# Optimization experiments

Hardware: AMD Instinct MI355X
Metric: run time of the kernel (lower is better)

## Reference

```python
import jax, jax.numpy as jnp
import numpy as np

H = 16   # num_heads
K = 2    # top_k experts per token


def _layer_norm(x, g, b, eps=1e-5):
    mu = jnp.mean(x, axis=-1, keepdims=True)
    var = jnp.mean(jnp.square(x - mu), axis=-1, keepdims=True)
    return (x - mu) * jax.lax.rsqrt(var + eps) * g + b


def setup_inputs() -> dict:
    key = jax.random.key(0)
    ks = jax.random.split(key, 8)
    B, S, D, E = 2, 2048, 1024, 8
    sc = 0.02
    return {
        "x": jax.random.normal(ks[0], (B, S, D), jnp.float32),
        "wq": jax.random.normal(ks[1], (D, D), jnp.float32) * sc,
        "wk": jax.random.normal(ks[2], (D, D), jnp.float32) * sc,
        "wv": jax.random.normal(ks[3], (D, D), jnp.float32) * sc,
        "wo": jax.random.normal(ks[4], (D, D), jnp.float32) * sc,
        "ln1_g": jnp.ones((D,), jnp.float32),
        "ln1_b": jnp.zeros((D,), jnp.float32),
        "ln2_g": jnp.ones((D,), jnp.float32),
        "ln2_b": jnp.zeros((D,), jnp.float32),
        "router_w": jax.random.normal(ks[5], (E, D), jnp.float32) * sc,
        "expert_w": jax.random.normal(ks[6], (E, D, D), jnp.float32) * sc,
    }


def reference(x, wq, wk, wv, wo, ln1_g, ln1_b, ln2_g, ln2_b, router_w, expert_w):
    B, S, D = x.shape
    E = expert_w.shape[0]
    hd = D // H

    # ---- attention sublayer: x = x + attn(norm1(x)) ----
    h = _layer_norm(x, ln1_g, ln1_b)
    q = (h @ wq.T).reshape(B, S, H, hd).transpose(0, 2, 1, 3)  # bhsd
    k = (h @ wk.T).reshape(B, S, H, hd).transpose(0, 2, 1, 3)
    v = (h @ wv.T).reshape(B, S, H, hd).transpose(0, 2, 1, 3)
    scores = jnp.einsum("bhqd,bhkd->bhqk", q, k) / jnp.sqrt(jnp.float32(hd))
    causal = jnp.tril(jnp.ones((S, S), dtype=bool))
    scores = jnp.where(causal, scores, jnp.finfo(scores.dtype).min)
    probs = jax.nn.softmax(scores, axis=-1)
    attn = jnp.einsum("bhqk,bhkd->bhqd", probs, v)
    attn = attn.transpose(0, 2, 1, 3).reshape(B, S, D) @ wo.T
    x = x + attn

    # ---- MoE sublayer: x = x + moe(norm2(x)) ----
    h2 = _layer_norm(x, ln2_g, ln2_b)
    logits = jnp.einsum("bsd,ed->bse", h2, router_w)          # [B,S,E]
    top_logits, top_ids = jax.lax.top_k(logits, K)            # [B,S,K]
    gates = jax.nn.softmax(top_logits, axis=-1)               # [B,S,K]
    # dense combine weights over experts (E is small): sum_k gate_k * onehot(id_k)
    combine = jnp.sum(jax.nn.one_hot(top_ids, E, dtype=h2.dtype) * gates[..., None], axis=-2)  # [B,S,E]
    # per-token matvec with expert weights: token @ W_e.T for each expert, then weighted sum
    y = jnp.einsum("bsd,eod->bseo", h2, expert_w)             # [B,S,E,D]
    moe_out = jnp.einsum("bse,bseo->bso", combine, y)
    return x + moe_out
```

## Files before the change

kernel.cpp:

```cpp
#include <hip/hip_runtime.h>
#include <hip/hip_bf16.h>
#include <cstdint>


typedef __bf16 bf16;
typedef __bf16 bf16x8 __attribute__((ext_vector_type(8)));
typedef __bf16 bf16x4 __attribute__((ext_vector_type(4)));
typedef float f32x4 __attribute__((ext_vector_type(4)));
typedef float f32x16 __attribute__((ext_vector_type(16)));

#define MFMA(a, b, c) __builtin_amdgcn_mfma_f32_16x16x32_bf16(a, b, c, 0, 0, 0)
#define MFMA32(a, b, c) __builtin_amdgcn_mfma_f32_32x32x16_bf16(a, b, c, 0, 0, 0)

__device__ __forceinline__ void gld16(void* lds, const void* g) {
  __builtin_amdgcn_global_load_lds(
      (const __attribute__((address_space(1))) void*)g,
      (__attribute__((address_space(3))) void*)lds, 16, 0, 0);
}

__global__ void prep_weights(const float* __restrict__ wq, const float* __restrict__ wk,
                             const float* __restrict__ wv, const float* __restrict__ wo,
                             const float* __restrict__ expw,
                             bf16* __restrict__ wqh, bf16* __restrict__ wql,
                             bf16* __restrict__ wkh, bf16* __restrict__ wkl,
                             bf16* __restrict__ wvh, bf16* __restrict__ wvl,
                             bf16* __restrict__ woh, bf16* __restrict__ wol,
                             bf16* __restrict__ ewh) {
  int bid = blockIdx.x;
  if (bid < 4096) {
    int wsel = bid >> 10;
    const float* src = wsel == 0 ? wq : wsel == 1 ? wk : wsel == 2 ? wv : wo;
    bf16* hi = wsel == 0 ? wqh : wsel == 1 ? wkh : wsel == 2 ? wvh : woh;
    bf16* lo = wsel == 0 ? wql : wsel == 1 ? wkl : wsel == 2 ? wvl : wol;
    int i = ((bid & 1023) * 256 + threadIdx.x) * 4;
    float4 v = *(const float4*)(src + i);
    float a[4] = {v.x, v.y, v.z, v.w};
#pragma unroll
    for (int j = 0; j < 4; j++) {
      bf16 h = (bf16)a[j];
      hi[i + j] = h;
      lo[i + j] = (bf16)(a[j] - (float)h);
    }
  } else {
    int i = ((bid - 4096) * 256 + threadIdx.x) * 4;
    float4 v = *(const float4*)(expw + i);
    ewh[i] = (bf16)v.x; ewh[i + 1] = (bf16)v.y;
    ewh[i + 2] = (bf16)v.z; ewh[i + 3] = (bf16)v.w;
  }
}

__global__ void ln_split(const float* __restrict__ x, const float* __restrict__ g,
                         const float* __restrict__ b, bf16* __restrict__ hi,
                         bf16* __restrict__ lo) {
  int tok = blockIdx.x, t = threadIdx.x;
  float4 v = ((const float4*)(x + (size_t)tok * 1024))[t];
  float s = v.x + v.y + v.z + v.w;
  float ss = v.x * v.x + v.y * v.y + v.z * v.z + v.w * v.w;
#pragma unroll
  for (int o = 1; o < 64; o <<= 1) { s += __shfl_xor(s, o); ss += __shfl_xor(ss, o); }
  __shared__ float red[8];
  int w = t >> 6, lane = t & 63;
  if (lane == 0) { red[w] = s; red[4 + w] = ss; }
  __syncthreads();
  s = red[0] + red[1] + red[2] + red[3];
  ss = red[4] + red[5] + red[6] + red[7];
  float mu = s * (1.f / 1024.f);
  float rstd = rsqrtf(ss * (1.f / 1024.f) - mu * mu + 1e-5f);
  float4 gv = ((const float4*)g)[t], bv = ((const float4*)b)[t];
  float y[4] = {(v.x - mu) * rstd * gv.x + bv.x, (v.y - mu) * rstd * gv.y + bv.y,
                (v.z - mu) * rstd * gv.z + bv.z, (v.w - mu) * rstd * gv.w + bv.w};
  size_t o = (size_t)tok * 1024 + t * 4;
#pragma unroll
  for (int j = 0; j < 4; j++) {
    bf16 h = (bf16)y[j];
    hi[o + j] = h;
    lo[o + j] = (bf16)(y[j] - (float)h);
  }
}

__global__ void ln2route(const float* __restrict__ x1, const float* __restrict__ g,
                         const float* __restrict__ b, const float* __restrict__ rw,
                         bf16* __restrict__ h2h, int* __restrict__ eid,
                         float2* __restrict__ gout) {
  int tok = blockIdx.x, t = threadIdx.x;
  float4 v = ((const float4*)(x1 + (size_t)tok * 1024))[t];
  float s = v.x + v.y + v.z + v.w;
  float ss = v.x * v.x + v.y * v.y + v.z * v.z + v.w * v.w;
#pragma unroll
  for (int o = 1; o < 64; o <<= 1) { s += __shfl_xor(s, o); ss += __shfl_xor(ss, o); }
  __shared__ float red[8];
  __shared__ float h2s[1024];
  __shared__ float lg[8];
  int w = t >> 6, lane = t & 63;
  if (lane == 0) { red[w] = s; red[4 + w] = ss; }
  __syncthreads();
  s = red[0] + red[1] + red[2] + red[3];
  ss = red[4] + red[5] + red[6] + red[7];
  float mu = s * (1.f / 1024.f);
  float rstd = rsqrtf(ss * (1.f / 1024.f) - mu * mu + 1e-5f);
  float4 gv = ((const float4*)g)[t], bv = ((const float4*)b)[t];
  float4 y;
  y.x = (v.x - mu) * rstd * gv.x + bv.x;
  y.y = (v.y - mu) * rstd * gv.y + bv.y;
  y.z = (v.z - mu) * rstd * gv.z + bv.z;
  y.w = (v.w - mu) * rstd * gv.w + bv.w;
  ((float4*)h2s)[t] = y;
  size_t o = (size_t)tok * 1024 + t * 4;
  h2h[o] = (bf16)y.x; h2h[o + 1] = (bf16)y.y;
  h2h[o + 2] = (bf16)y.z; h2h[o + 3] = (bf16)y.w;
  __syncthreads();
  float a0 = 0.f, a1 = 0.f;
  const float4* r0 = (const float4*)(rw + (2 * w) * 1024);
  const float4* r1 = (const float4*)(rw + (2 * w + 1) * 1024);
#pragma unroll
  for (int it = 0; it < 4; it++) {
    float4 xv = ((const float4*)h2s)[lane + 64 * it];
    float4 w0 = r0[lane + 64 * it];
    float4 w1 = r1[lane + 64 * it];
    a0 += xv.x * w0.x + xv.y * w0.y + xv.z * w0.z + xv.w * w0.w;
    a1 += xv.x * w1.x + xv.y * w1.y + xv.z * w1.z + xv.w * w1.w;
  }
#pragma unroll
  for (int o2 = 1; o2 < 64; o2 <<= 1) {
    a0 += __shfl_xor(a0, o2);
    a1 += __shfl_xor(a1, o2);
  }
  if (lane == 0) { lg[2 * w] = a0; lg[2 * w + 1] = a1; }
  __syncthreads();
  if (t == 0) {
    int i0 = 0; float l0 = lg[0];
#pragma unroll
    for (int e = 1; e < 8; e++) if (lg[e] > l0) { l0 = lg[e]; i0 = e; }
    int i1 = -1; float l1 = -3e38f;
#pragma unroll
    for (int e = 0; e < 8; e++) if (e != i0 && lg[e] > l1) { l1 = lg[e]; i1 = e; }
    float e1 = __expf(l1 - l0);
    float den = 1.f + e1;
    eid[tok] = i0 | (i1 << 4);
    gout[tok] = make_float2(1.f / den, e1 / den);
  }
}

__global__ void build_lists(const int* __restrict__ eid,
                            const float2* __restrict__ gv,
                            int* __restrict__ tlist, float* __restrict__ glist,
                            int* __restrict__ cnt) {
  int e = blockIdx.x, t = threadIdx.x;
  int lane = t & 63, w = t >> 6;
  __shared__ int wt[4];
  int base = 0;
  for (int c = 0; c < 16; c++) {
    int tok = c * 256 + t;
    int pair = eid[tok];
    int e0 = pair & 15, e1 = pair >> 4;
    bool p = (e0 == e) || (e1 == e);
    float2 g2 = gv[tok];
    float gate = (e0 == e) ? g2.x : g2.y;
    unsigned long long m = __ballot(p);
    int rank = __popcll(m & ((1ull << lane) - 1ull));
    if (lane == 0) wt[w] = __popcll(m);
    __syncthreads();
    int off = base;
    for (int i = 0; i < w; i++) off += wt[i];
    if (p) {
      tlist[e * 4096 + off + rank] = tok;
      glist[e * 4096 + off + rank] = gate;
    }
    base += wt[0] + wt[1] + wt[2] + wt[3];
    __syncthreads();
  }
  if (t == 0) cnt[e] = base;
  int pad = (base + 127) & ~127;
  if (pad > 4096) pad = 4096;
  for (int i = base + t; i < pad; i += 256) {
    tlist[e * 4096 + i] = 0;
    glist[e * 4096 + i] = 0.f;
  }
}

__device__ __forceinline__ void gemm_core_split(
    const bf16* __restrict__ Ah, const bf16* __restrict__ Al,
    const bf16* __restrict__ Bh, const bf16* __restrict__ Bl, int m0, int n0,
    f32x4 (&acc)[4][4]) {
  __shared__ __align__(16) bf16 As_h[4096], As_l[4096], Bs_h[4096], Bs_l[4096];
  int t = threadIdx.x, lane = t & 63, w = t >> 6;
  int i0 = t, i1 = t + 256;
  const bf16* a0h = Ah + (size_t)(m0 + (i0 >> 2)) * 1024 + (i0 & 3) * 8;
  const bf16* a1h = Ah + (size_t)(m0 + (i1 >> 2)) * 1024 + (i1 & 3) * 8;
  const bf16* a0l = Al + (size_t)(m0 + (i0 >> 2)) * 1024 + (i0 & 3) * 8;
  const bf16* a1l = Al + (size_t)(m0 + (i1 >> 2)) * 1024 + (i1 & 3) * 8;
  const bf16* b0h = Bh + (size_t)(n0 + (i0 >> 2)) * 1024 + (i0 & 3) * 8;
  const bf16* b1h = Bh + (size_t)(n0 + (i1 >> 2)) * 1024 + (i1 & 3) * 8;
  const bf16* b0l = Bl + (size_t)(n0 + (i0 >> 2)) * 1024 + (i0 & 3) * 8;
  const bf16* b1l = Bl + (size_t)(n0 + (i1 >> 2)) * 1024 + (i1 & 3) * 8;
  int wm = (w >> 1) * 64, wn = (w & 1) * 64;
  int lr = lane & 15, lq = lane >> 4;
  for (int k0 = 0; k0 < 1024; k0 += 32) {
    __syncthreads();
    gld16(&As_h[i0 * 8], a0h + k0); gld16(&As_h[i1 * 8], a1h + k0);
    gld16(&As_l[i0 * 8], a0l + k0); gld16(&As_l[i1 * 8], a1l + k0);
    gld16(&Bs_h[i0 * 8], b0h + k0); gld16(&Bs_h[i1 * 8], b1h + k0);
    gld16(&Bs_l[i0 * 8], b0l + k0); gld16(&Bs_l[i1 * 8], b1l + k0);
    __syncthreads();
    bf16x8 ah[4], al4[4], bh[4], bl4[4];
#pragma unroll
    for (int i = 0; i < 4; i++) {
      ah[i]  = *(const bf16x8*)&As_h[(wm + i * 16 + lr) * 32 + lq * 8];
      al4[i] = *(const bf16x8*)&As_l[(wm + i * 16 + lr) * 32 + lq * 8];
      bh[i]  = *(const bf16x8*)&Bs_h[(wn + i * 16 + lr) * 32 + lq * 8];
      bl4[i] = *(const bf16x8*)&Bs_l[(wn + i * 16 + lr) * 32 + lq * 8];
    }
#pragma unroll
    for (int i = 0; i < 4; i++)
#pragma unroll
      for (int j = 0; j < 4; j++) {
        f32x4 c = acc[i][j];
        c = MFMA(ah[i], bh[j], c);
        c = MFMA(ah[i], bl4[j], c);
        c = MFMA(al4[i], bh[j], c);
        acc[i][j] = c;
      }
  }
}

__global__ __launch_bounds__(256, 2) void gemm_qkv(
    const bf16* __restrict__ hh, const bf16* __restrict__ hl,
    const bf16* __restrict__ wqh, const bf16* __restrict__ wql,
    const bf16* __restrict__ wkh, const bf16* __restrict__ wkl,
    const bf16* __restrict__ wvh, const bf16* __restrict__ wvl,
    bf16* __restrict__ qh, bf16* __restrict__ ql, bf16* __restrict__ kh,
    bf16* __restrict__ kl, bf16* __restrict__ vth, bf16* __restrict__ vtl) {
  int n0 = blockIdx.x * 128, m0 = blockIdx.y * 128, z = blockIdx.z;
  const bf16 *Bh = wqh, *Bl = wql;
  if (z == 1) { Bh = wkh; Bl = wkl; }
  if (z == 2) { Bh = wvh; Bl = wvl; }
  f32x4 acc[4][4];
#pragma unroll
  for (int i = 0; i < 4; i++)
#pragma unroll
    for (int j = 0; j < 4; j++) acc[i][j] = (f32x4){0.f, 0.f, 0.f, 0.f};
  gemm_core_split(hh, hl, Bh, Bl, m0, n0, acc);
  int t = threadIdx.x, lane = t & 63, w = t >> 6;
  int wm = (w >> 1) * 64, wn = (w & 1) * 64, lr = lane & 15, lq = lane >> 4;
  if (z < 2) {
    bf16* Oh = z == 0 ? qh : kh;
    bf16* Ol = z == 0 ? ql : kl;
    float scale = (z == 0) ? (0.125f * 1.44269504f) : 1.0f;
#pragma unroll
    for (int i = 0; i < 4; i++)
#pragma unroll
      for (int j = 0; j < 4; j++)
#pragma unroll
        for (int r = 0; r < 4; r++) {
          size_t row = m0 + wm + i * 16 + lq * 4 + r;
          int col = n0 + wn + j * 16 + lr;
          float v = acc[i][j][r] * scale;
          bf16 h = (bf16)v;
          Oh[row * 1024 + col] = h;
          Ol[row * 1024 + col] = (bf16)(v - (float)h);
        }
  } else {
    int bb = m0 >> 11;
    int srow0 = m0 & 2047;
#pragma unroll
    for (int i = 0; i < 4; i++)
#pragma unroll
      for (int j = 0; j < 4; j++) {
        int col = n0 + wn + j * 16 + lr;
        int head = col >> 6, d = col & 63;
        int s = srow0 + wm + i * 16 + lq * 4;
        bf16x4 hv, lv;
#pragma unroll
        for (int r = 0; r < 4; r++) {
          float v = acc[i][j][r];
          bf16 h = (bf16)v;
          hv[r] = h;
          lv[r] = (bf16)(v - (float)h);
        }
        size_t off = ((size_t)((bb * 16 + head) * 64 + d)) * 2048 + s;
        *(bf16x4*)(vth + off) = hv;
        *(bf16x4*)(vtl + off) = lv;
      }
  }
}

__global__ __launch_bounds__(256, 2) void gemm_wo(
    const bf16* __restrict__ ah, const bf16* __restrict__ al,
    const bf16* __restrict__ bh, const bf16* __restrict__ bl,
    const float* __restrict__ resid, float* __restrict__ outp) {
  int n0 = blockIdx.x * 128, m0 = blockIdx.y * 128;
  f32x4 acc[4][4];
#pragma unroll
  for (int i = 0; i < 4; i++)
#pragma unroll
    for (int j = 0; j < 4; j++) acc[i][j] = (f32x4){0.f, 0.f, 0.f, 0.f};
  gemm_core_split(ah, al, bh, bl, m0, n0, acc);
  int t = threadIdx.x, lane = t & 63, w = t >> 6;
  int wm = (w >> 1) * 64, wn = (w & 1) * 64, lr = lane & 15, lq = lane >> 4;
#pragma unroll
  for (int i = 0; i < 4; i++)
#pragma unroll
    for (int j = 0; j < 4; j++)
#pragma unroll
      for (int r = 0; r < 4; r++) {
        size_t row = m0 + wm + i * 16 + lq * 4 + r;
        int col = n0 + wn + j * 16 + lr;
        outp[row * 1024 + col] = resid[row * 1024 + col] + acc[i][j][r];
      }
}

__global__ __launch_bounds__(256, 2) void attn_fused(
    const bf16* __restrict__ qh, const bf16* __restrict__ ql,
    const bf16* __restrict__ kh, const bf16* __restrict__ kl,
    const bf16* __restrict__ vth, const bf16* __restrict__ vtl,
    bf16* __restrict__ oh, bf16* __restrict__ ol) {
  const int S = 2048, D = 1024;
  int qt = 15 - blockIdx.y;
  int hb = blockIdx.x;
  int head = hb & 15, b = hb >> 4;
  int qb = qt * 128;
  int t = threadIdx.x, lane = t & 63, w = t >> 6;
  int l31 = lane & 31, l5 = lane >> 5;
  int base = b * S, hcol = head * 64;

  __shared__ __align__(16) bf16 Kh_s[2][4096], Kl_s[2][4096];
  __shared__ __align__(16) bf16 Vh_s[2][4096], Vl_s[2][4096];
  __shared__ float Ls[128];

  bf16x8 qfh[4], qfl[4];
  {
    const bf16* p1 = qh + (size_t)(base + qb + w * 32 + l31) * D + hcol + l5 * 8;
    const bf16* p2 = ql + (size_t)(base + qb + w * 32 + l31) * D + hcol + l5 * 8;
#pragma unroll
    for (int c = 0; c < 4; c++) {
      qfh[c] = *(const bf16x8*)(p1 + 16 * c);
      qfl[c] = *(const bf16x8*)(p2 + 16 * c);
    }
  }
  f32x16 O0, O1;
  float lsum = 0.f;
#pragma unroll
  for (int r = 0; r < 16; r++) { O0[r] = 0.f; O1[r] = 0.f; }

  int r0 = t >> 3, p0 = t & 7;
  int g0 = p0 ^ (r0 & 7);
  const bf16* k0hp = kh + (size_t)(base + r0) * D + hcol + g0 * 8;
  const bf16* k1hp = kh + (size_t)(base + 32 + r0) * D + hcol + g0 * 8;
  const bf16* k0lp = kl + (size_t)(base + r0) * D + hcol + g0 * 8;
  const bf16* k1lp = kl + (size_t)(base + 32 + r0) * D + hcol + g0 * 8;
  const bf16* v0hp = vth + (size_t)(hb * 64 + r0) * 2048 + g0 * 8;
  const bf16* v1hp = vth + (size_t)(hb * 64 + 32 + r0) * 2048 + g0 * 8;
  const bf16* v0lp = vtl + (size_t)(hb * 64 + r0) * 2048 + g0 * 8;
  const bf16* v1lp = vtl + (size_t)(hb * 64 + 32 + r0) * 2048 + g0 * 8;

  int qwmin = qb + w * 32;
  int nt = 2 * qt + 2;

#define STAGE(kts, bb) do { \
    gld16(&Kh_s[bb][t * 8], k0hp + (size_t)(kts) * D); \
    gld16(&Kh_s[bb][2048 + t * 8], k1hp + (size_t)(kts) * D); \
    gld16(&Kl_s[bb][t * 8], k0lp + (size_t)(kts) * D); \
    gld16(&Kl_s[bb][2048 + t * 8], k1lp + (size_t)(kts) * D); \
    gld16(&Vh_s[bb][t * 8], v0hp + (kts)); \
    gld16(&Vh_s[bb][2048 + t * 8], v1hp + (kts)); \
    gld16(&Vl_s[bb][t * 8], v0lp + (kts)); \
    gld16(&Vl_s[bb][2048 + t * 8], v1lp + (kts)); \
  } while (0)

  STAGE(0, 0);
  __syncthreads();

  for (int ti = 0; ti < nt; ti++) {
    int kt = ti * 64;
    int bb = ti & 1;
    if (ti + 1 < nt) STAGE((ti + 1) * 64, bb ^ 1);
    if (kt <= qwmin + 31) {
      bool skip1 = (kt + 32 > qwmin + 31);
#pragma unroll
      for (int ktile = 0; ktile < 2; ktile++) {
        if (ktile == 1 && skip1) break;
        bool maskt = (kt + 32 * ktile + 31 > qwmin);
        int keyr = ktile * 32 + l31;
        f32x16 sc;
#pragma unroll
        for (int r = 0; r < 16; r++) sc[r] = 0.f;
        __builtin_amdgcn_s_setprio(1);
#pragma unroll
        for (int c = 0; c < 4; c++) {
          int dg = ((2 * c + l5) ^ (keyr & 7)) * 8;
          bf16x8 kv = *(const bf16x8*)&Kh_s[bb][keyr * 64 + dg];
          bf16x8 km = *(const bf16x8*)&Kl_s[bb][keyr * 64 + dg];
          sc = MFMA32(kv, qfh[c], sc);
          sc = MFMA32(kv, qfl[c], sc);
          sc = MFMA32(km, qfh[c], sc);
        }
        __builtin_amdgcn_s_setprio(0);
        int kb0 = kt + 32 * ktile + 4 * l5;
        int qg = qwmin + l31;
        float pvv[16];
#pragma unroll
        for (int r = 0; r < 16; r++) {
          int cst = (r & 3) + 8 * (r >> 2);
          float sv = sc[r];
          if (maskt && (kb0 + cst > qg)) sv = -30000.f;
          float p = __builtin_amdgcn_exp2f(sv);
          pvv[r] = p;
          lsum += p;
        }
        uint32_t hw[4][2], lw[4][2];
#pragma unroll
        for (int o = 0; o < 4; o++)
#pragma unroll
          for (int j = 0; j < 2; j++) {
            int ra = 4 * o + 2 * j;
            bf16 h0 = (bf16)pvv[ra], h1 = (bf16)pvv[ra + 1];
            union { bf16 h[2]; uint32_t u; } ph, pl;
            ph.h[0] = h0; ph.h[1] = h1;
            pl.h[0] = (bf16)(pvv[ra] - (float)h0);
            pl.h[1] = (bf16)(pvv[ra + 1] - (float)h1);
            hw[o][j] = ph.u;
            lw[o][j] = pl.u;
          }
#pragma unroll
        for (int c2 = 0; c2 < 2; c2++) {
          union { uint32_t u[4]; bf16x8 v; } pa, plo;
          pa.u[0] = hw[2 * c2][0];     pa.u[1] = hw[2 * c2][1];
          pa.u[2] = hw[2 * c2 + 1][0]; pa.u[3] = hw[2 * c2 + 1][1];
          plo.u[0] = lw[2 * c2][0];     plo.u[1] = lw[2 * c2][1];
          plo.u[2] = lw[2 * c2 + 1][0]; plo.u[3] = lw[2 * c2 + 1][1];
          __builtin_amdgcn_s_setprio(1);
#pragma unroll
          for (int dtile = 0; dtile < 2; dtile++) {
            int d = dtile * 32 + l31;
            int gA = ((4 * ktile + 2 * c2) ^ (d & 7)) * 8 + 4 * l5;
            int gB = ((4 * ktile + 2 * c2 + 1) ^ (d & 7)) * 8 + 4 * l5;
            union { bf16x4 q[2]; bf16x8 v; } vbu, vmu;
            vbu.q[0] = *(const bf16x4*)&Vh_s[bb][d * 64 + gA];
            vbu.q[1] = *(const bf16x4*)&Vh_s[bb][d * 64 + gB];
            vmu.q[0] = *(const bf16x4*)&Vl_s[bb][d * 64 + gA];
            vmu.q[1] = *(const bf16x4*)&Vl_s[bb][d * 64 + gB];
            if (dtile == 0) {
              O0 = MFMA32(pa.v, vbu.v, O0);
              O0 = MFMA32(plo.v, vbu.v, O0);
              O0 = MFMA32(pa.v, vmu.v, O0);
            } else {
              O1 = MFMA32(pa.v, vbu.v, O1);
              O1 = MFMA32(plo.v, vbu.v, O1);
              O1 = MFMA32(pa.v, vmu.v, O1);
            }
          }
          __builtin_amdgcn_s_setprio(0);
        }
      }
    }
    __syncthreads();
  }
#undef STAGE
  float ltot = lsum + __shfl_xor(lsum, 32);
  if (lane < 32) Ls[w * 32 + l31] = ltot;
#pragma unroll
  for (int r = 0; r < 16; r++) {
    int qlocal = (r & 3) + 8 * (r >> 2) + 4 * l5;
    float linv = 1.f / Ls[w * 32 + qlocal];
    size_t tok = (size_t)(base + qb + w * 32 + qlocal);
    float v0 = O0[r] * linv;
    float v1 = O1[r] * linv;
    bf16 h0 = (bf16)v0, h1 = (bf16)v1;
    oh[tok * D + hcol + l31] = h0;
    ol[tok * D + hcol + l31] = (bf16)(v0 - (float)h0);
    oh[tok * D + hcol + 32 + l31] = h1;
    ol[tok * D + hcol + 32 + l31] = (bf16)(v1 - (float)h1);
  }
}

__global__ __launch_bounds__(256, 2) void gemm_moe(
    const bf16* __restrict__ A, const bf16* __restrict__ W,
    const int* __restrict__ tlist, const float* __restrict__ glist,
    const int* __restrict__ cnt, float* __restrict__ outp) {
  int e = blockIdx.z;
  int count = cnt[e];
  int m0 = blockIdx.y * 128;
  if (m0 >= count) return;
  int n0 = blockIdx.x * 128;
  const int* tl = tlist + e * 4096;
  const bf16* B = W + (size_t)e * 1024 * 1024;
  __shared__ __align__(16) bf16 As[4096], Bs[4096];
  int t = threadIdx.x, lane = t & 63, w = t >> 6;
  int i0 = t, i1 = t + 256;
  int ra = tl[m0 + (i0 >> 2)], rb = tl[m0 + (i1 >> 2)];
  const bf16* a0 = A + (size_t)ra * 1024 + (i0 & 3) * 8;
  const bf16* a1 = A + (size_t)rb * 1024 + (i1 & 3) * 8;
  const bf16* b0 = B + (size_t)(n0 + (i0 >> 2)) * 1024 + (i0 & 3) * 8;
  const bf16* b1 = B + (size_t)(n0 + (i1 >> 2)) * 1024 + (i1 & 3) * 8;
  int wm = (w >> 1) * 64, wn = (w & 1) * 64, lr = lane & 15, lq = lane >> 4;
  f32x4 acc[4][4];
#pragma unroll
  for (int i = 0; i < 4; i++)
#pragma unroll
    for (int j = 0; j < 4; j++) acc[i][j] = (f32x4){0.f, 0.f, 0.f, 0.f};
  for (int k0 = 0; k0 < 1024; k0 += 32) {
    __syncthreads();
    gld16(&As[i0 * 8], a0 + k0); gld16(&As[i1 * 8], a1 + k0);
    gld16(&Bs[i0 * 8], b0 + k0); gld16(&Bs[i1 * 8], b1 + k0);
    __syncthreads();
    bf16x8 af[4], bfr[4];
#pragma unroll
    for (int i = 0; i < 4; i++) {
      af[i] = *(const bf16x8*)&As[(wm + i * 16 + lr) * 32 + lq * 8];
      bfr[i] = *(const bf16x8*)&Bs[(wn + i * 16 + lr) * 32 + lq * 8];
    }
#pragma unroll
    for (int i = 0; i < 4; i++)
#pragma unroll
      for (int j = 0; j < 4; j++) acc[i][j] = MFMA(af[i], bfr[j], acc[i][j]);
  }
#pragma unroll
  for (int i = 0; i < 4; i++)
#pragma unroll
    for (int r = 0; r < 4; r++) {
      int slot = m0 + wm + i * 16 + lq * 4 + r;
      if (slot < count) {
        int tok = tl[slot];
        float gte = glist[e * 4096 + slot];
#pragma unroll
        for (int j = 0; j < 4; j++) {
          int col = n0 + wn + j * 16 + lr;
          atomicAdd(&outp[(size_t)tok * 1024 + col], gte * acc[i][j][r]);
        }
      }
    }
}

extern "C" void kernel_launch(void* const* d_in, const int* in_sizes, int n_in,
                              void* d_out, int out_size, void* d_ws, size_t ws_size,
                              hipStream_t stream) {
  (void)in_sizes; (void)n_in; (void)out_size; (void)ws_size;
  const float* x    = (const float*)d_in[0];
  const float* wq   = (const float*)d_in[1];
  const float* wk   = (const float*)d_in[2];
  const float* wv   = (const float*)d_in[3];
  const float* wo   = (const float*)d_in[4];
  const float* ln1g = (const float*)d_in[5];
  const float* ln1b = (const float*)d_in[6];
  const float* ln2g = (const float*)d_in[7];
  const float* ln2b = (const float*)d_in[8];
  const float* rw   = (const float*)d_in[9];
  const float* expw = (const float*)d_in[10];
  float* out = (float*)d_out;

  char* p = (char*)d_ws;
  auto take = [&](size_t bytes) -> char* {
    char* r = p;
    p += (bytes + 255) & ~(size_t)255;
    return r;
  };
  const size_t ND2 = 4096ull * 1024 * 2;
  const size_t WD2 = 1024ull * 1024 * 2;
  bf16* h_hi = (bf16*)take(ND2); bf16* h_lo = (bf16*)take(ND2);
  bf16* wqh = (bf16*)take(WD2); bf16* wql = (bf16*)take(WD2);
  bf16* wkh = (bf16*)take(WD2); bf16* wkl = (bf16*)take(WD2);
  bf16* wvh = (bf16*)take(WD2); bf16* wvl = (bf16*)take(WD2);
  bf16* woh = (bf16*)take(WD2); bf16* wol = (bf16*)take(WD2);
  bf16* q_hi = (bf16*)take(ND2); bf16* q_lo = (bf16*)take(ND2);
  bf16* k_hi = (bf16*)take(ND2); bf16* k_lo = (bf16*)take(ND2);
  bf16* vt_hi = (bf16*)take(ND2); bf16* vt_lo = (bf16*)take(ND2);
  bf16* a_hi = (bf16*)take(ND2); bf16* a_lo = (bf16*)take(ND2);
  bf16* h2h  = (bf16*)take(ND2);
  bf16* ewh  = (bf16*)take(8ull * 1024 * 1024 * 2);
  int*   tlist  = (int*)take(8ull * 4096 * 4);
  float* glist  = (float*)take(8ull * 4096 * 4);
  int*   cnt    = (int*)take(64);
  int*   reid   = (int*)take(4096 * 4);
  float2* rg    = (float2*)take(4096 * 8);

  prep_weights<<<12288, 256, 0, stream>>>(wq, wk, wv, wo, expw, wqh, wql, wkh,
                                          wkl, wvh, wvl, woh, wol, ewh);
  ln_split<<<4096, 256, 0, stream>>>(x, ln1g, ln1b, h_hi, h_lo);
  gemm_qkv<<<dim3(8, 32, 3), 256, 0, stream>>>(h_hi, h_lo, wqh, wql, wkh, wkl,
                                               wvh, wvl, q_hi, q_lo, k_hi, k_lo,
                                               vt_hi, vt_lo);
  attn_fused<<<dim3(32, 16), 256, 0, stream>>>(q_hi, q_lo, k_hi, k_lo, vt_hi,
                                               vt_lo, a_hi, a_lo);
  gemm_wo<<<dim3(8, 32), 256, 0, stream>>>(a_hi, a_lo, woh, wol, x, out);
  ln2route<<<4096, 256, 0, stream>>>(out, ln2g, ln2b, rw, h2h, reid, rg);
  build_lists<<<8, 256, 0, stream>>>(reid, rg, tlist, glist, cnt);
  gemm_moe<<<dim3(8, 32, 8), 256, 0, stream>>>(h2h, ewh, tlist, glist, cnt,
                                               out);
}
```

Before: 417.7 us.

## Drop low-precision split for V projection and attention PV product

The V projection moves to a separate single-precision bf16 GEMM (one MFMA per tile instead of three). The V low-part buffer, its loads and its staging are removed from attention, cutting PV MFMAs from three to two and halving V LDS traffic. V is stored with a new XOR swizzle on 4-element groups, and QK scores are split into two independent accumulators to shorten the MFMA dependency chain. The cost is lower accuracy in V and the attention output, since the bf16 residual correction for V is dropped.

```diff
diff --git a/kernel.cpp b/kernel.cpp
--- a/kernel.cpp
+++ b/kernel.cpp
@@ -223,17 +223,15 @@
   }
 }
 
-__global__ __launch_bounds__(256, 2) void gemm_qkv(
+__global__ __launch_bounds__(256, 2) void gemm_qk(
     const bf16* __restrict__ hh, const bf16* __restrict__ hl,
     const bf16* __restrict__ wqh, const bf16* __restrict__ wql,
     const bf16* __restrict__ wkh, const bf16* __restrict__ wkl,
-    const bf16* __restrict__ wvh, const bf16* __restrict__ wvl,
     bf16* __restrict__ qh, bf16* __restrict__ ql, bf16* __restrict__ kh,
-    bf16* __restrict__ kl, bf16* __restrict__ vth, bf16* __restrict__ vtl) {
+    bf16* __restrict__ kl) {
   int n0 = blockIdx.x * 128, m0 = blockIdx.y * 128, z = blockIdx.z;
-  const bf16 *Bh = wqh, *Bl = wql;
-  if (z == 1) { Bh = wkh; Bl = wkl; }
-  if (z == 2) { Bh = wvh; Bl = wvl; }
+  const bf16* Bh = z ? wkh : wqh;
+  const bf16* Bl = z ? wkl : wql;
   f32x4 acc[4][4];
 #pragma unroll
   for (int i = 0; i < 4; i++)
@@ -242,46 +240,73 @@
   gemm_core_split(hh, hl, Bh, Bl, m0, n0, acc);
   int t = threadIdx.x, lane = t & 63, w = t >> 6;
   int wm = (w >> 1) * 64, wn = (w & 1) * 64, lr = lane & 15, lq = lane >> 4;
-  if (z < 2) {
-    bf16* Oh = z == 0 ? qh : kh;
-    bf16* Ol = z == 0 ? ql : kl;
-    float scale = (z == 0) ? (0.125f * 1.44269504f) : 1.0f;
+  bf16* Oh = z ? kh : qh;
+  bf16* Ol = z ? kl : ql;
+  float scale = z ? 1.0f : (0.125f * 1.44269504f);
+#pragma unroll
+  for (int i = 0; i < 4; i++)
+#pragma unroll
+    for (int j = 0; j < 4; j++)
+#pragma unroll
+      for (int r = 0; r < 4; r++) {
+        size_t row = m0 + wm + i * 16 + lq * 4 + r;
+        int col = n0 + wn + j * 16 + lr;
+        float v = acc[i][j][r] * scale;
+        bf16 h = (bf16)v;
+        Oh[row * 1024 + col] = h;
+        Ol[row * 1024 + col] = (bf16)(v - (float)h);
+      }
+}
+
+__global__ __launch_bounds__(256, 2) void gemm_v(
+    const bf16* __restrict__ A, const bf16* __restrict__ B,
+    bf16* __restrict__ vth) {
+  int n0 = blockIdx.x * 128, m0 = blockIdx.y * 128;
+  __shared__ __align__(16) bf16 As[4096], Bs[4096];
+  int t = threadIdx.x, lane = t & 63, w = t >> 6;
+  int i0 = t, i1 = t + 256;
+  const bf16* a0 = A + (size_t)(m0 + (i0 >> 2)) * 1024 + (i0 & 3) * 8;
+  const bf16* a1 = A + (size_t)(m0 + (i1 >> 2)) * 1024 + (i1 & 3) * 8;
+  const bf16* b0 = B + (size_t)(n0 + (i0 >> 2)) * 1024 + (i0 & 3) * 8;
+  const bf16* b1 = B + (size_t)(n0 + (i1 >> 2)) * 1024 + (i1 & 3) * 8;
+  int wm = (w >> 1) * 64, wn = (w & 1) * 64, lr = lane & 15, lq = lane >> 4;
+  f32x4 acc[4][4];
+#pragma unroll
+  for (int i = 0; i < 4; i++)
+#pragma unroll
+    for (int j = 0; j < 4; j++) acc[i][j] = (f32x4){0.f, 0.f, 0.f, 0.f};
+  for (int k0 = 0; k0 < 1024; k0 += 32) {
+    __syncthreads();
+    gld16(&As[i0 * 8], a0 + k0); gld16(&As[i1 * 8], a1 + k0);
+    gld16(&Bs[i0 * 8], b0 + k0); gld16(&Bs[i1 * 8], b1 + k0);
+    __syncthreads();
+    bf16x8 af[4], bfr[4];
+#pragma unroll
+    for (int i = 0; i < 4; i++) {
+      af[i] = *(const bf16x8*)&As[(wm + i * 16 + lr) * 32 + lq * 8];
+      bfr[i] = *(const bf16x8*)&Bs[(wn + i * 16 + lr) * 32 + lq * 8];
+    }
 #pragma unroll
     for (int i = 0; i < 4; i++)
 #pragma unroll
-      for (int j = 0; j < 4; j++)
-#pragma unroll
-        for (int r = 0; r < 4; r++) {
-          size_t row = m0 + wm + i * 16 + lq * 4 + r;
-          int col = n0 + wn + j * 16 + lr;
-          float v = acc[i][j][r] * scale;
-          bf16 h = (bf16)v;
-          Oh[row * 1024 + col] = h;
-          Ol[row * 1024 + col] = (bf16)(v - (float)h);
-        }
-  } else {
-    int bb = m0 >> 11;
-    int srow0 = m0 & 2047;
-#pragma unroll
-    for (int i = 0; i < 4; i++)
-#pragma unroll
-      for (int j = 0; j < 4; j++) {
-        int col = n0 + wn + j * 16 + lr;
-        int head = col >> 6, d = col & 63;
-        int s = srow0 + wm + i * 16 + lq * 4;
-        bf16x4 hv, lv;
-#pragma unroll
-        for (int r = 0; r < 4; r++) {
-          float v = acc[i][j][r];
-          bf16 h = (bf16)v;
-          hv[r] = h;
-          lv[r] = (bf16)(v - (float)h);
-        }
-        size_t off = ((size_t)((bb * 16 + head) * 64 + d)) * 2048 + s;
-        *(bf16x4*)(vth + off) = hv;
-        *(bf16x4*)(vtl + off) = lv;
-      }
-  }
+      for (int j = 0; j < 4; j++) acc[i][j] = MFMA(af[i], bfr[j], acc[i][j]);
+  }
+  int bb = m0 >> 11;
+  int srow0 = m0 & 2047;
+#pragma unroll
+  for (int i = 0; i < 4; i++)
+#pragma unroll
+    for (int j = 0; j < 4; j++) {
+      int col = n0 + wn + j * 16 + lr;
+      int head = col >> 6, d = col & 63;
+      int s = srow0 + wm + i * 16 + lq * 4;
+      int ss = (s & ~63) | (((((s >> 2) & 15)) ^ (d & 15)) << 2);
+      bf16x4 hv;
+#pragma unroll
+      for (int r = 0; r < 4; r++) hv[r] = (bf16)acc[i][j][r];
+      size_t off = ((size_t)((bb * 16 + head) * 64 + d)) * 2048 + ss;
+      *(bf16x4*)(vth + off) = hv;
+    }
 }
 
 __global__ __launch_bounds__(256, 2) void gemm_wo(
@@ -312,7 +337,7 @@
 __global__ __launch_bounds__(256, 2) void attn_fused(
     const bf16* __restrict__ qh, const bf16* __restrict__ ql,
     const bf16* __restrict__ kh, const bf16* __restrict__ kl,
-    const bf16* __restrict__ vth, const bf16* __restrict__ vtl,
+    const bf16* __restrict__ vth,
     bf16* __restrict__ oh, bf16* __restrict__ ol) {
   const int S = 2048, D = 1024;
   int qt = 15 - blockIdx.y;
@@ -324,7 +349,7 @@
   int base = b * S, hcol = head * 64;
 
   __shared__ __align__(16) bf16 Kh_s[2][4096], Kl_s[2][4096];
-  __shared__ __align__(16) bf16 Vh_s[2][4096], Vl_s[2][4096];
+  __shared__ __align__(16) bf16 Vh_s[2][4096];
   __shared__ float Ls[128];
 
   bf16x8 qfh[4], qfl[4];
@@ -348,10 +373,8 @@
   const bf16* k1hp = kh + (size_t)(base + 32 + r0) * D + hcol + g0 * 8;
   const bf16* k0lp = kl + (size_t)(base + r0) * D + hcol + g0 * 8;
   const bf16* k1lp = kl + (size_t)(base + 32 + r0) * D + hcol + g0 * 8;
-  const bf16* v0hp = vth + (size_t)(hb * 64 + r0) * 2048 + g0 * 8;
-  const bf16* v1hp = vth + (size_t)(hb * 64 + 32 + r0) * 2048 + g0 * 8;
-  const bf16* v0lp = vtl + (size_t)(hb * 64 + r0) * 2048 + g0 * 8;
-  const bf16* v1lp = vtl + (size_t)(hb * 64 + 32 + r0) * 2048 + g0 * 8;
+  const bf16* v0hp = vth + (size_t)(hb * 64 + r0) * 2048 + p0 * 8;
+  const bf16* v1hp = vth + (size_t)(hb * 64 + 32 + r0) * 2048 + p0 * 8;
 
   int qwmin = qb + w * 32;
   int nt = 2 * qt + 2;
@@ -363,8 +386,6 @@
     gld16(&Kl_s[bb][2048 + t * 8], k1lp + (size_t)(kts) * D); \
     gld16(&Vh_s[bb][t * 8], v0hp + (kts)); \
     gld16(&Vh_s[bb][2048 + t * 8], v1hp + (kts)); \
-    gld16(&Vl_s[bb][t * 8], v0lp + (kts)); \
-    gld16(&Vl_s[bb][2048 + t * 8], v1lp + (kts)); \
   } while (0)
 
   STAGE(0, 0);
@@ -381,18 +402,24 @@
         if (ktile == 1 && skip1) break;
         bool maskt = (kt + 32 * ktile + 31 > qwmin);
         int keyr = ktile * 32 + l31;
-        f32x16 sc;
-#pragma unroll
-        for (int r = 0; r < 16; r++) sc[r] = 0.f;
+        f32x16 scA, scB;
+#pragma unroll
+        for (int r = 0; r < 16; r++) { scA[r] = 0.f; scB[r] = 0.f; }
         __builtin_amdgcn_s_setprio(1);
 #pragma unroll
         for (int c = 0; c < 4; c++) {
           int dg = ((2 * c + l5) ^ (keyr & 7)) * 8;
           bf16x8 kv = *(const bf16x8*)&Kh_s[bb][keyr * 64 + dg];
           bf16x8 km = *(const bf16x8*)&Kl_s[bb][keyr * 64 + dg];
-          sc = MFMA32(kv, qfh[c], sc);
-          sc = MFMA32(kv, qfl[c], sc);
-          sc = MFMA32(km, qfh[c], sc);
+          if (c < 2) {
+            scA = MFMA32(kv, qfh[c], scA);
+            scA = MFMA32(kv, qfl[c], scA);
+            scA = MFMA32(km, qfh[c], scA);
+          } else {
+            scB = MFMA32(kv, qfh[c], scB);
+            scB = MFMA32(kv, qfl[c], scB);
+            scB = MFMA32(km, qfh[c], scB);
+          }
         }
         __builtin_amdgcn_s_setprio(0);
         int kb0 = kt + 32 * ktile + 4 * l5;
@@ -401,7 +428,7 @@
 #pragma unroll
         for (int r = 0; r < 16; r++) {
           int cst = (r & 3) + 8 * (r >> 2);
-          float sv = sc[r];
+          float sv = scA[r] + scB[r];
           if (maskt && (kb0 + cst > qg)) sv = -30000.f;
           float p = __builtin_amdgcn_exp2f(sv);
           pvv[r] = p;
@@ -432,21 +459,16 @@
 #pragma unroll
           for (int dtile = 0; dtile < 2; dtile++) {
             int d = dtile * 32 + l31;
-            int gA = ((4 * ktile + 2 * c2) ^ (d & 7)) * 8 + 4 * l5;
-            int gB = ((4 * ktile + 2 * c2 + 1) ^ (d & 7)) * 8 + 4 * l5;
-            union { bf16x4 q[2]; bf16x8 v; } vbu, vmu;
-            vbu.q[0] = *(const bf16x4*)&Vh_s[bb][d * 64 + gA];
-            vbu.q[1] = *(const bf16x4*)&Vh_s[bb][d * 64 + gB];
-            vmu.q[0] = *(const bf16x4*)&Vl_s[bb][d * 64 + gA];
-            vmu.q[1] = *(const bf16x4*)&Vl_s[bb][d * 64 + gB];
+            int pqA = ((8 * ktile + 4 * c2 + l5) ^ (d & 15)) * 4;
+            union { bf16x4 q[2]; bf16x8 v; } vbu;
+            vbu.q[0] = *(const bf16x4*)&Vh_s[bb][d * 64 + pqA];
+            vbu.q[1] = *(const bf16x4*)&Vh_s[bb][d * 64 + (pqA ^ 8)];
             if (dtile == 0) {
               O0 = MFMA32(pa.v, vbu.v, O0);
               O0 = MFMA32(plo.v, vbu.v, O0);
-              O0 = MFMA32(pa.v, vmu.v, O0);
             } else {
               O1 = MFMA32(pa.v, vbu.v, O1);
               O1 = MFMA32(plo.v, vbu.v, O1);
-              O1 = MFMA32(pa.v, vmu.v, O1);
             }
           }
           __builtin_amdgcn_s_setprio(0);
@@ -563,7 +585,7 @@
   bf16* woh = (bf16*)take(WD2); bf16* wol = (bf16*)take(WD2);
   bf16* q_hi = (bf16*)take(ND2); bf16* q_lo = (bf16*)take(ND2);
   bf16* k_hi = (bf16*)take(ND2); bf16* k_lo = (bf16*)take(ND2);
-  bf16* vt_hi = (bf16*)take(ND2); bf16* vt_lo = (bf16*)take(ND2);
+  bf16* vt_hi = (bf16*)take(ND2);
   bf16* a_hi = (bf16*)take(ND2); bf16* a_lo = (bf16*)take(ND2);
   bf16* h2h  = (bf16*)take(ND2);
   bf16* ewh  = (bf16*)take(8ull * 1024 * 1024 * 2);
@@ -576,11 +598,11 @@
   prep_weights<<<12288, 256, 0, stream>>>(wq, wk, wv, wo, expw, wqh, wql, wkh,
                                           wkl, wvh, wvl, woh, wol, ewh);
   ln_split<<<4096, 256, 0, stream>>>(x, ln1g, ln1b, h_hi, h_lo);
-  gemm_qkv<<<dim3(8, 32, 3), 256, 0, stream>>>(h_hi, h_lo, wqh, wql, wkh, wkl,
-                                               wvh, wvl, q_hi, q_lo, k_hi, k_lo,
-                                               vt_hi, vt_lo);
+  gemm_qk<<<dim3(8, 32, 2), 256, 0, stream>>>(h_hi, h_lo, wqh, wql, wkh, wkl,
+                                              q_hi, q_lo, k_hi, k_lo);
+  gemm_v<<<dim3(8, 32), 256, 0, stream>>>(h_hi, wvh, vt_hi);
   attn_fused<<<dim3(32, 16), 256, 0, stream>>>(q_hi, q_lo, k_hi, k_lo, vt_hi,
-                                               vt_lo, a_hi, a_lo);
+                                               a_hi, a_lo);
   gemm_wo<<<dim3(8, 32), 256, 0, stream>>>(a_hi, a_lo, woh, wol, x, out);
   ln2route<<<4096, 256, 0, stream>>>(out, ln2g, ln2b, rw, h2h, reid, rg);
   build_lists<<<8, 256, 0, stream>>>(reid, rg, tlist, glist, cnt);
```

After: 418.1 us. No clear change (+0.1%).
